# Kernel optimization log

Hardware: AMD Instinct MI355X
Metric: run time of the kernel (lower is better)

Reference implementation:

```python
import jax, jax.numpy as jnp
import numpy as np

HIDDEN = 1024
HEADS = 16
HEAD_DIM = HIDDEN // HEADS
B, T = 4, 2048


def setup_inputs() -> dict:
    key = jax.random.key(0)
    k_x, k_w1, k_b1, k_w2, k_b2 = jax.random.split(key, 5)
    lim1 = 1.0 / np.sqrt(HIDDEN)
    x = jax.random.normal(k_x, (B, T, HIDDEN), dtype=jnp.float32)
    # causal lower-triangular mask, broadcastable to [B, H, T, T]
    mask = jnp.tril(jnp.ones((T, T), dtype=jnp.int32))[None, None, :, :]
    # qkv_proj: Linear(HIDDEN, 3*HIDDEN); torch Linear: y = x @ W.T + b
    W_qkv = jax.random.uniform(k_w1, (3 * HIDDEN, HIDDEN), minval=-lim1, maxval=lim1, dtype=jnp.float32)
    b_qkv = jax.random.uniform(k_b1, (3 * HIDDEN,), minval=-lim1, maxval=lim1, dtype=jnp.float32)
    W_out = jax.random.uniform(k_w2, (HIDDEN, HIDDEN), minval=-lim1, maxval=lim1, dtype=jnp.float32)
    b_out = jax.random.uniform(k_b2, (HIDDEN,), minval=-lim1, maxval=lim1, dtype=jnp.float32)
    return {"x": x, "mask": mask, "W_qkv": W_qkv, "b_qkv": b_qkv, "W_out": W_out, "b_out": b_out}


def reference(x, mask, W_qkv, b_qkv, W_out, b_out):
    Bx, Tx, C = x.shape
    qkv = x @ W_qkv.T + b_qkv                      # [B, T, 3C]
    qkv = qkv.reshape(Bx, Tx, 3, HEADS, HEAD_DIM)
    qkv = jnp.transpose(qkv, (2, 0, 3, 1, 4))      # [3, B, H, T, Dh]
    Q, K, V = qkv[0], qkv[1], qkv[2]
    scale = 1.0 / np.sqrt(HEAD_DIM)
    scores = jnp.einsum('bhqd,bhkd->bhqk', Q, K) * scale  # [B, H, T, T]
    scores = jnp.where(mask == 0, -jnp.inf, scores)
    probs = jax.nn.softmax(scores, axis=-1)
    ctx = jnp.einsum('bhqk,bhkd->bhqd', probs, V)  # [B, H, T, Dh]
    ctx = jnp.transpose(ctx, (0, 2, 1, 3)).reshape(Bx, Tx, C)
    return ctx @ W_out.T + b_out
```

## Files before the change

### kernel.cpp

```cpp
#include <hip/hip_runtime.h>
#include <cstdint>
#include <cstddef>

#define B_ 4
#define T_ 2048
#define C_ 1024
#define H_ 16
#define D_ 64

typedef __attribute__((ext_vector_type(8))) __bf16 bf16x8;
typedef __attribute__((ext_vector_type(4))) float floatx4;

#define QSCL (0.125f * 1.44269504088896f)
#define FMAX 24.0f

__device__ __forceinline__ unsigned short f2bf(float f) {
  union { float f; unsigned int u; } v; v.f = f;
  unsigned int r = v.u + 0x7fffu + ((v.u >> 16) & 1u);
  return (unsigned short)(r >> 16);
}
__device__ __forceinline__ ushort4 pk4(float a, float b, float c, float d) {
  ushort4 u; u.x = f2bf(a); u.y = f2bf(b); u.z = f2bf(c); u.w = f2bf(d);
  return u;
}
__device__ __forceinline__ bf16x8 cvt8(float4 a, float4 b) {
  bf16x8 r;
  r[0] = a.x; r[1] = a.y; r[2] = a.z; r[3] = a.w;
  r[4] = b.x; r[5] = b.y; r[6] = b.z; r[7] = b.w;
  return r;
}

__device__ __forceinline__ void gl_lds16(const void* g, void* l) {
  __builtin_amdgcn_global_load_lds(
      (const __attribute__((address_space(1))) unsigned int*)g,
      (__attribute__((address_space(3))) unsigned int*)l, 16, 0, 0);
}

__global__ __launch_bounds__(256)
void conv_bf16(const float* __restrict__ src, unsigned short* __restrict__ dst,
               int n8) {
  for (int i = blockIdx.x * 256 + threadIdx.x; i < n8; i += gridDim.x * 256) {
    const float4* s = (const float4*)src + 2 * (size_t)i;
    float4 a = s[0], b = s[1];
    ((bf16x8*)dst)[i] = cvt8(a, b);
  }
}

template<int EPI, int GATHER, int WBF>
__global__ __launch_bounds__(256, 3)
void gemm_bt(const unsigned short* __restrict__ Abf,
             const void* __restrict__ Wraw,
             const float* __restrict__ bias,
             float* __restrict__ out,
             unsigned short* __restrict__ qws,
             unsigned short* __restrict__ kws,
             unsigned short* __restrict__ vtws)
{
  alignas(16) __shared__ unsigned short As[128 * 64];
  alignas(16) __shared__ unsigned short Bs[WBF ? 128 * 64 : 128 * 72];
  const int tid  = threadIdx.x;
  const int lane = tid & 63;
  const int wid  = tid >> 6;
  const int col  = lane & 15;
  const int quad = lane >> 4;
  const int wm = (wid >> 1) << 6;
  const int wn = (wid & 1) << 6;
  const int bm = blockIdx.y << 7;
  const int bn = blockIdx.x << 7;

  const float* Wf          = (const float*)Wraw;
  const unsigned short* Wb = (const unsigned short*)Wraw;

  const int r0 = tid >> 3;
  const int c0 = tid & 7;

  floatx4 acc[4][4];
#pragma unroll
  for (int i = 0; i < 4; ++i)
#pragma unroll
    for (int j = 0; j < 4; ++j)
      acc[i][j] = (floatx4){0.f, 0.f, 0.f, 0.f};

  for (int k0 = 0; k0 < 1024; k0 += 64) {
    __syncthreads();
#pragma unroll
    for (int s = 0; s < 4; ++s) {
      const int row  = (s << 5) + r0;
      const int colE = ((c0 ^ (row & 7)) << 3);
      const unsigned short* gsrc;
      if (GATHER) {
        const int m = bm + row;
        const int b = m >> 11, t = m & 2047;
        const int h = k0 >> 6;
        gsrc = Abf + ((((size_t)(b * 16 + h) << 11) + t) << 6) + colE;
      } else {
        gsrc = Abf + (size_t)(bm + row) * 1024 + k0 + colE;
      }
      gl_lds16(gsrc, (char*)As + (s << 12) + (wid << 10));
    }
    if (WBF) {
#pragma unroll
      for (int s = 0; s < 4; ++s) {
        const int row  = (s << 5) + r0;
        const int colE = ((c0 ^ (row & 7)) << 3);
        const unsigned short* gsrc = Wb + (size_t)(bn + row) * 1024 + k0 + colE;
        gl_lds16(gsrc, (char*)Bs + (s << 12) + (wid << 10));
      }
    } else {
#pragma unroll
      for (int s = 0; s < 4; ++s) {
        const int row = (s << 5) + r0;
        const int kc  = c0 << 3;
        const float* wsrc = &Wf[(size_t)(bn + row) * 1024 + k0 + kc];
        float4 w0 = *(const float4*)wsrc;
        float4 w1 = *(const float4*)(wsrc + 4);
        *(bf16x8*)&Bs[row * 72 + kc] = cvt8(w0, w1);
      }
    }
    __syncthreads();
#pragma unroll
    for (int kk = 0; kk < 64; kk += 32) {
      bf16x8 af[4], bfr[4];
#pragma unroll
      for (int i = 0; i < 4; ++i) {
        const int r = wm + i * 16 + col;
        af[i] = *(const bf16x8*)&As[(r << 6) + ((kk + quad * 8) ^ ((r & 7) << 3))];
      }
#pragma unroll
      for (int j = 0; j < 4; ++j) {
        const int r = wn + j * 16 + col;
        if (WBF)
          bfr[j] = *(const bf16x8*)&Bs[(r << 6) + ((kk + quad * 8) ^ ((r & 7) << 3))];
        else
          bfr[j] = *(const bf16x8*)&Bs[r * 72 + kk + quad * 8];
      }
#pragma unroll
      for (int i = 0; i < 4; ++i)
#pragma unroll
        for (int j = 0; j < 4; ++j)
          acc[i][j] = __builtin_amdgcn_mfma_f32_16x16x32_bf16(af[i], bfr[j], acc[i][j], 0, 0, 0);
    }
  }

#pragma unroll
  for (int i = 0; i < 4; ++i) {
    const int row = bm + wm + i * 16 + quad * 4;
#pragma unroll
    for (int j = 0; j < 4; ++j) {
      const int n  = bn + wn + j * 16 + col;
      const float bv = bias[n];
      float v[4];
#pragma unroll
      for (int r = 0; r < 4; ++r) v[r] = acc[i][j][r] + bv;

      if (EPI == 1) {
#pragma unroll
        for (int r = 0; r < 4; ++r)
          out[(size_t)(row + r) * 1024 + n] = v[r];
      } else {
        const int s   = n >> 10;
        const int rem = n & 1023;
        const int h   = rem >> 6;
        const int d   = rem & 63;
        const int b   = row >> 11;
        const int t   = row & 2047;
        const size_t bh = (size_t)(b * H_ + h);
        if (s == 0) {
#pragma unroll
          for (int r = 0; r < 4; ++r)
            qws[(bh * T_ + t + r) * D_ + d] = f2bf(v[r] * QSCL);
        } else if (s == 1) {
#pragma unroll
          for (int r = 0; r < 4; ++r)
            kws[(bh * T_ + t + r) * D_ + d] = f2bf(v[r]);
        } else {
          *(ushort4*)&vtws[(bh * D_ + d) * T_ + t] = pk4(v[0], v[1], v[2], v[3]);
        }
      }
    }
  }
}

__global__ __launch_bounds__(256)
void attn_causal(unsigned short* __restrict__ qws,
                 const unsigned short* __restrict__ kws,
                 const unsigned short* __restrict__ vtws)
{
  alignas(16) __shared__ unsigned short Ks[2][64][72];
  alignas(16) __shared__ unsigned short Vs[2][64][72];
  alignas(16) __shared__ unsigned short Ps[4][16][72];
  const int tid  = threadIdx.x;
  const int lane = tid & 63;
  const int wid  = tid >> 6;
  const int col  = lane & 15;
  const int quad = lane >> 4;

  const int bh   = blockIdx.x & 63;
  const int pr   = blockIdx.x >> 6;

  const unsigned short* Kp  = kws + (size_t)bh * T_ * D_;
  const unsigned short* Vtp = vtws + (size_t)bh * D_ * T_;

  const int srow = tid >> 3;
  const int scol = (tid & 7) << 3;

#pragma unroll
  for (int half = 0; half < 2; ++half) {
    const int band = (half == 0) ? pr : (31 - pr);
    const int nk   = band + 1;
    const int q0   = (band << 6) + (wid << 4);
    unsigned short* Qp = qws + ((size_t)bh * T_ + q0) * D_;

    const bf16x8 bq0 = *(const bf16x8*)&Qp[col * D_ + quad * 8];
    const bf16x8 bq1 = *(const bf16x8*)&Qp[col * D_ + 32 + quad * 8];

    floatx4 o[4];
#pragma unroll
    for (int j = 0; j < 4; ++j) o[j] = (floatx4){0.f, 0.f, 0.f, 0.f};
    float lrow = 0.f;

    {
      uint4 ka = *(const uint4*)&Kp[(size_t)srow * D_ + scol];
      uint4 kb = *(const uint4*)&Kp[(size_t)(srow + 32) * D_ + scol];
      uint4 va = *(const uint4*)&Vtp[(size_t)srow * T_ + scol];
      uint4 vb = *(const uint4*)&Vtp[(size_t)(srow + 32) * T_ + scol];
      *(uint4*)&Ks[0][srow][scol]      = ka;
      *(uint4*)&Ks[0][srow + 32][scol] = kb;
      *(uint4*)&Vs[0][srow][scol]      = va;
      *(uint4*)&Vs[0][srow + 32][scol] = vb;
      __syncthreads();
    }

    for (int kt = 0; kt < nk; ++kt) {
      const int buf = kt & 1;

      uint4 ka, kb, va, vb;
      const bool more = (kt + 1 < nk);
      if (more) {
        const int kn = (kt + 1) << 6;
        ka = *(const uint4*)&Kp[(size_t)(kn + srow) * D_ + scol];
        kb = *(const uint4*)&Kp[(size_t)(kn + srow + 32) * D_ + scol];
        va = *(const uint4*)&Vtp[(size_t)srow * T_ + kn + scol];
        vb = *(const uint4*)&Vtp[(size_t)(srow + 32) * T_ + kn + scol];
      }

      floatx4 s[4];
#pragma unroll
      for (int g = 0; g < 4; ++g) {
        const bf16x8 kA = *(const bf16x8*)&Ks[buf][g * 16 + col][quad * 8];
        const bf16x8 kB = *(const bf16x8*)&Ks[buf][g * 16 + col][32 + quad * 8];
        s[g] = (floatx4){0.f, 0.f, 0.f, 0.f};
        s[g] = __builtin_amdgcn_mfma_f32_16x16x32_bf16(kA, bq0, s[g], 0, 0, 0);
        s[g] = __builtin_amdgcn_mfma_f32_16x16x32_bf16(kB, bq1, s[g], 0, 0, 0);
      }

      if (kt == nk - 1) {
        const int lim = (wid << 4) + col;
#pragma unroll
        for (int g = 0; g < 4; ++g)
#pragma unroll
          for (int r = 0; r < 4; ++r)
            if (g * 16 + quad * 4 + r > lim) s[g][r] = -1e30f;
      }

#pragma unroll
      for (int g = 0; g < 4; ++g)
#pragma unroll
        for (int r = 0; r < 4; ++r)
          s[g][r] = exp2f(s[g][r] - FMAX);
      lrow += ((s[0][0] + s[0][1]) + (s[0][2] + s[0][3])) +
              ((s[1][0] + s[1][1]) + (s[1][2] + s[1][3])) +
              ((s[2][0] + s[2][1]) + (s[2][2] + s[2][3])) +
              ((s[3][0] + s[3][1]) + (s[3][2] + s[3][3]));

#pragma unroll
      for (int g = 0; g < 4; ++g)
        *(ushort4*)&Ps[wid][col][g * 16 + quad * 4] =
            pk4(s[g][0], s[g][1], s[g][2], s[g][3]);
      asm volatile("s_waitcnt lgkmcnt(0)" ::: "memory");
      const bf16x8 ap0 = *(const bf16x8*)&Ps[wid][col][quad * 8];
      const bf16x8 ap1 = *(const bf16x8*)&Ps[wid][col][32 + quad * 8];

#pragma unroll
      for (int j = 0; j < 4; ++j) {
        const bf16x8 vA = *(const bf16x8*)&Vs[buf][j * 16 + col][quad * 8];
        const bf16x8 vB = *(const bf16x8*)&Vs[buf][j * 16 + col][32 + quad * 8];
        o[j] = __builtin_amdgcn_mfma_f32_16x16x32_bf16(ap0, vA, o[j], 0, 0, 0);
        o[j] = __builtin_amdgcn_mfma_f32_16x16x32_bf16(ap1, vB, o[j], 0, 0, 0);
      }

      __syncthreads();
      if (more) {
        const int nb = buf ^ 1;
        *(uint4*)&Ks[nb][srow][scol]      = ka;
        *(uint4*)&Ks[nb][srow + 32][scol] = kb;
        *(uint4*)&Vs[nb][srow][scol]      = va;
        *(uint4*)&Vs[nb][srow + 32][scol] = vb;
      }
      __syncthreads();
    }

    lrow += __shfl_xor(lrow, 16);
    lrow += __shfl_xor(lrow, 32);
    float lr[4];
#pragma unroll
    for (int r = 0; r < 4; ++r) lr[r] = 1.0f / __shfl(lrow, quad * 4 + r);
#pragma unroll
    for (int j = 0; j < 4; ++j)
#pragma unroll
      for (int r = 0; r < 4; ++r)
        Qp[(size_t)(quad * 4 + r) * D_ + j * 16 + col] = f2bf(o[j][r] * lr[r]);
  }
}

extern "C" void kernel_launch(void* const* d_in, const int* in_sizes, int n_in,
                              void* d_out, int out_size, void* d_ws, size_t ws_size,
                              hipStream_t stream) {
  const float* x     = (const float*)d_in[0];
  const float* W_qkv = (const float*)d_in[2];
  const float* b_qkv = (const float*)d_in[3];
  const float* W_out = (const float*)d_in[4];
  const float* b_out = (const float*)d_in[5];
  float* out = (float*)d_out;

  const size_t per = (size_t)B_ * H_ * T_ * D_;
  unsigned short* qws  = (unsigned short*)d_ws;
  unsigned short* vtws = qws + per;
  unsigned short* kws  = (unsigned short*)d_out;
  unsigned short* xbf  = kws + per;

  conv_bf16<<<dim3(2048), 256, 0, stream>>>(x, xbf, (int)(per >> 3));

  gemm_bt<0, 0, 0><<<dim3(3072 / 128, 8192 / 128), 256, 0, stream>>>(
      xbf, (const void*)W_qkv, b_qkv, nullptr, qws, kws, vtws);

  attn_causal<<<dim3(16 * 64), 256, 0, stream>>>(qws, kws, vtws);

  conv_bf16<<<dim3(512), 256, 0, stream>>>(W_out, vtws, (C_ * C_) >> 3);

  gemm_bt<1, 1, 1><<<dim3(1024 / 128, 8192 / 128), 256, 0, stream>>>(
      qws, (const void*)vtws, b_out, out, nullptr, nullptr, nullptr);
}
```

Before: 299.1 us.

## Load K/V fragments directly from global memory, drop LDS staging and barriers

The attention kernel stops staging K and V tiles in double-buffered shared memory. Each wave now loads its MFMA operand fragments straight from global memory, relying on L1/L2 to serve the reuse across the four waves. This removes both block-wide __syncthreads per key tile and frees shared memory. In exchange the kernel loses explicit prefetch overlap and issues four times the global load traffic per block. It also adds a launch-bounds occupancy hint and switches the probability packing to native bf16 conversion.

```diff
diff --git a/kernel.cpp b/kernel.cpp
--- a/kernel.cpp
+++ b/kernel.cpp
@@ -28,6 +28,11 @@
   r[0] = a.x; r[1] = a.y; r[2] = a.z; r[3] = a.w;
   r[4] = b.x; r[5] = b.y; r[6] = b.z; r[7] = b.w;
   return r;
+}
+__device__ __forceinline__ ushort4 pk4c(float a, float b, float c, float d) {
+  union { __bf16 b4[4]; ushort4 u; } w;
+  w.b4[0] = (__bf16)a; w.b4[1] = (__bf16)b; w.b4[2] = (__bf16)c; w.b4[3] = (__bf16)d;
+  return w.u;
 }
 
 __device__ __forceinline__ void gl_lds16(const void* g, void* l) {
@@ -181,13 +186,11 @@
   }
 }
 
-__global__ __launch_bounds__(256)
+__global__ __launch_bounds__(256, 3)
 void attn_causal(unsigned short* __restrict__ qws,
                  const unsigned short* __restrict__ kws,
                  const unsigned short* __restrict__ vtws)
 {
-  alignas(16) __shared__ unsigned short Ks[2][64][72];
-  alignas(16) __shared__ unsigned short Vs[2][64][72];
   alignas(16) __shared__ unsigned short Ps[4][16][72];
   const int tid  = threadIdx.x;
   const int lane = tid & 63;
@@ -198,11 +201,8 @@
   const int bh   = blockIdx.x & 63;
   const int pr   = blockIdx.x >> 6;
 
-  const unsigned short* Kp  = kws + (size_t)bh * T_ * D_;
-  const unsigned short* Vtp = vtws + (size_t)bh * D_ * T_;
-
-  const int srow = tid >> 3;
-  const int scol = (tid & 7) << 3;
+  const unsigned short* kp = kws + (size_t)bh * T_ * D_ + (size_t)col * D_ + quad * 8;
+  const unsigned short* vp = vtws + (size_t)bh * D_ * T_ + (size_t)col * T_ + quad * 8;
 
 #pragma unroll
   for (int half = 0; half < 2; ++half) {
@@ -219,39 +219,22 @@
     for (int j = 0; j < 4; ++j) o[j] = (floatx4){0.f, 0.f, 0.f, 0.f};
     float lrow = 0.f;
 
-    {
-      uint4 ka = *(const uint4*)&Kp[(size_t)srow * D_ + scol];
-      uint4 kb = *(const uint4*)&Kp[(size_t)(srow + 32) * D_ + scol];
-      uint4 va = *(const uint4*)&Vtp[(size_t)srow * T_ + scol];
-      uint4 vb = *(const uint4*)&Vtp[(size_t)(srow + 32) * T_ + scol];
-      *(uint4*)&Ks[0][srow][scol]      = ka;
-      *(uint4*)&Ks[0][srow + 32][scol] = kb;
-      *(uint4*)&Vs[0][srow][scol]      = va;
-      *(uint4*)&Vs[0][srow + 32][scol] = vb;
-      __syncthreads();
-    }
-
     for (int kt = 0; kt < nk; ++kt) {
-      const int buf = kt & 1;
-
-      uint4 ka, kb, va, vb;
-      const bool more = (kt + 1 < nk);
-      if (more) {
-        const int kn = (kt + 1) << 6;
-        ka = *(const uint4*)&Kp[(size_t)(kn + srow) * D_ + scol];
-        kb = *(const uint4*)&Kp[(size_t)(kn + srow + 32) * D_ + scol];
-        va = *(const uint4*)&Vtp[(size_t)srow * T_ + kn + scol];
-        vb = *(const uint4*)&Vtp[(size_t)(srow + 32) * T_ + kn + scol];
+      const unsigned short* kbase = kp + (size_t)kt * 4096;
+
+      bf16x8 kA[4], kB[4];
+#pragma unroll
+      for (int g = 0; g < 4; ++g) {
+        kA[g] = *(const bf16x8*)(kbase + g * 1024);
+        kB[g] = *(const bf16x8*)(kbase + g * 1024 + 32);
       }
 
       floatx4 s[4];
 #pragma unroll
       for (int g = 0; g < 4; ++g) {
-        const bf16x8 kA = *(const bf16x8*)&Ks[buf][g * 16 + col][quad * 8];
-        const bf16x8 kB = *(const bf16x8*)&Ks[buf][g * 16 + col][32 + quad * 8];
         s[g] = (floatx4){0.f, 0.f, 0.f, 0.f};
-        s[g] = __builtin_amdgcn_mfma_f32_16x16x32_bf16(kA, bq0, s[g], 0, 0, 0);
-        s[g] = __builtin_amdgcn_mfma_f32_16x16x32_bf16(kB, bq1, s[g], 0, 0, 0);
+        s[g] = __builtin_amdgcn_mfma_f32_16x16x32_bf16(kA[g], bq0, s[g], 0, 0, 0);
+        s[g] = __builtin_amdgcn_mfma_f32_16x16x32_bf16(kB[g], bq1, s[g], 0, 0, 0);
       }
 
       if (kt == nk - 1) {
@@ -276,28 +259,23 @@
 #pragma unroll
       for (int g = 0; g < 4; ++g)
         *(ushort4*)&Ps[wid][col][g * 16 + quad * 4] =
-            pk4(s[g][0], s[g][1], s[g][2], s[g][3]);
+            pk4c(s[g][0], s[g][1], s[g][2], s[g][3]);
       asm volatile("s_waitcnt lgkmcnt(0)" ::: "memory");
       const bf16x8 ap0 = *(const bf16x8*)&Ps[wid][col][quad * 8];
       const bf16x8 ap1 = *(const bf16x8*)&Ps[wid][col][32 + quad * 8];
 
+      const unsigned short* vbase = vp + (size_t)kt * 64;
+      bf16x8 vA[4], vB[4];
 #pragma unroll
       for (int j = 0; j < 4; ++j) {
-        const bf16x8 vA = *(const bf16x8*)&Vs[buf][j * 16 + col][quad * 8];
-        const bf16x8 vB = *(const bf16x8*)&Vs[buf][j * 16 + col][32 + quad * 8];
-        o[j] = __builtin_amdgcn_mfma_f32_16x16x32_bf16(ap0, vA, o[j], 0, 0, 0);
-        o[j] = __builtin_amdgcn_mfma_f32_16x16x32_bf16(ap1, vB, o[j], 0, 0, 0);
-      }
-
-      __syncthreads();
-      if (more) {
-        const int nb = buf ^ 1;
-        *(uint4*)&Ks[nb][srow][scol]      = ka;
-        *(uint4*)&Ks[nb][srow + 32][scol] = kb;
-        *(uint4*)&Vs[nb][srow][scol]      = va;
-        *(uint4*)&Vs[nb][srow + 32][scol] = vb;
-      }
-      __syncthreads();
+        vA[j] = *(const bf16x8*)(vbase + (size_t)j * 32768);
+        vB[j] = *(const bf16x8*)(vbase + (size_t)j * 32768 + 32);
+      }
+#pragma unroll
+      for (int j = 0; j < 4; ++j) {
+        o[j] = __builtin_amdgcn_mfma_f32_16x16x32_bf16(ap0, vA[j], o[j], 0, 0, 0);
+        o[j] = __builtin_amdgcn_mfma_f32_16x16x32_bf16(ap1, vB[j], o[j], 0, 0, 0);
+      }
     }
 
     lrow += __shfl_xor(lrow, 16);
```

Measured after the change: 435.1 us. +45.5%, slower.
